# Performance work log

Measured on AMD Instinct MI355X. Metric: run time of the kernel, lower is better.

The kernel has to match this reference:

```python
import jax, jax.numpy as jnp
import numpy as np

N_AFFINES = 4
N_SDFS = 4
BATCH = 8192
DEPTH = 6


def setup_inputs() -> dict:
    key = jax.random.key(0)
    k1, k2, k3, k4, k5, k6, k7 = jax.random.split(key, 7)
    query = jax.random.normal(k1, (BATCH, 2), dtype=jnp.float32)
    # Contractive affines: scale*rotation + translation (homogeneous 3x3), guaranteed invertible.
    theta = jax.random.uniform(k2, (N_AFFINES,), minval=0.0, maxval=2.0 * np.pi)
    s = 0.4 + 0.2 * jax.random.uniform(k3, (N_AFFINES,))  # contraction factors in [0.4, 0.6]
    t = 0.4 * jax.random.normal(k4, (N_AFFINES, 2))
    c, sn = jnp.cos(theta), jnp.sin(theta)
    row0 = jnp.stack([s * c, -s * sn, t[:, 0]], axis=-1)
    row1 = jnp.stack([s * sn, s * c, t[:, 1]], axis=-1)
    row2 = jnp.broadcast_to(jnp.array([0.0, 0.0, 1.0]), (N_AFFINES, 3))
    affine_mats = jnp.stack([row0, row1, row2], axis=1).astype(jnp.float32)  # (N,3,3)
    sdf_centers = 0.5 * jax.random.normal(k5, (N_SDFS, 2), dtype=jnp.float32)
    sdf_radii = (0.3 + 0.2 * jax.random.uniform(k6, (N_SDFS,))).astype(jnp.float32)
    return {
        "query": query,
        "affine_scales": s.astype(jnp.float32),
        "affine_mats": affine_mats,
        "sdf_centers": sdf_centers,
        "sdf_radii": sdf_radii,
        "depth": DEPTH,
    }


def reference(query, affine_scales, affine_mats, sdf_centers, sdf_radii, depth):
    # back transforms: inverse matrices and reciprocal scales
    back_scales = 1.0 / affine_scales              # (N,)
    back_mats = jnp.linalg.inv(affine_mats)        # (N,3,3)

    # Compose all N^depth transform combinations (mirrors the nested list comprehension).
    Tm = jnp.eye(3, dtype=jnp.float32)[None]       # (1,3,3)
    sc = jnp.ones((1,), dtype=jnp.float32)         # (1,)
    for _ in range(depth):
        Tm = jnp.einsum('aij,njk->anik', Tm, back_mats).reshape(-1, 3, 3)
        sc = (sc[:, None] * back_scales[None, :]).reshape(-1)
    # Tm: (T,3,3), sc: (T,) with T = N^depth

    B = query.shape[0]
    qpad = jnp.concatenate([query, jnp.ones((B, 1), dtype=query.dtype)], axis=1)  # (B,3)
    qt = jnp.einsum('tij,bj->tbi', Tm, qpad)[..., :2]  # (T,B,2)

    # Circle SDFs: ||p - center|| - radius, batched over all K sdfs -> (T,K,B)
    diff = qt[:, None, :, :] - sdf_centers[None, :, None, :]
    d = jnp.sqrt(jnp.sum(diff * diff, axis=-1)) - sdf_radii[None, :, None]
    d = d / sc[:, None, None]  # 1/scale * sdf(...)

    return jnp.min(jnp.min(d, axis=0), axis=0)  # (B,)
```

## Files before the change

kernel.cpp:

```cpp
#include <hip/hip_runtime.h>
#include <math.h>


#define NA 4
#define T_TOTAL 4096
#define BATCH 8192
#define TPB 256
#define TCHUNK 64
#define NCHUNK 64

__device__ __forceinline__ float fsqrt(float x) { return __builtin_amdgcn_sqrtf(x); }

__constant__ unsigned char LO_COMBO[64] = {
    0, 21, 42, 63,
    1, 4, 16,   2, 8, 32,   3, 12, 48,
    20, 17, 5,  22, 25, 37, 23, 29, 53,
    40, 34, 10, 41, 38, 26, 43, 46, 58,
    60, 51, 15, 61, 55, 31, 62, 59, 47,
    6, 9, 18, 24, 33, 36,
    7, 13, 19, 28, 49, 52,
    11, 14, 35, 44, 50, 56,
    27, 30, 39, 45, 54, 57
};


__device__ __forceinline__ void compute_inverses(const float* __restrict__ mats,
                                                 const float* __restrict__ scales,
                                                 float (*inv)[8], int tid) {
    if (tid < NA) {
        const int n = tid;
        float a = mats[n * 9 + 0], b = mats[n * 9 + 1], e = mats[n * 9 + 2];
        float c = mats[n * 9 + 3], d = mats[n * 9 + 4], f = mats[n * 9 + 5];
        float rd = 1.0f / (a * d - b * c);
        float i00 = d * rd, i01 = -b * rd, i10 = -c * rd, i11 = a * rd;
        inv[n][0] = i00; inv[n][1] = i01; inv[n][2] = i10; inv[n][3] = i11;
        inv[n][4] = -(i00 * e + i01 * f);
        inv[n][5] = -(i10 * e + i11 * f);
        inv[n][6] = scales[n];
        inv[n][7] = 0.0f;
    }
}

__device__ __forceinline__ void gen_transforms(const float (*inv)[8], float4 (*xf)[4],
                                               int hi, int tid, int nthreads,
                                               const float* __restrict__ centers,
                                               const float* __restrict__ radii) {
    for (int i = tid; i < TCHUNK; i += nthreads) {
        int t = hi * 64 + (int)LO_COMBO[i];
        int dg = (t >> 10) & 3;
        float m00 = inv[dg][0], m01 = inv[dg][1], m10 = inv[dg][2], m11 = inv[dg][3];
        float tx = inv[dg][4], ty = inv[dg][5], sp = inv[dg][6];
        #pragma unroll
        for (int s = 8; s >= 0; s -= 2) {
            dg = (t >> s) & 3;
            float b00 = inv[dg][0], b01 = inv[dg][1], b10 = inv[dg][2], b11 = inv[dg][3];
            float bx = inv[dg][4], by = inv[dg][5];
            float n00 = fmaf(m00, b00, m01 * b10);
            float n01 = fmaf(m00, b01, m01 * b11);
            float n10 = fmaf(m10, b00, m11 * b10);
            float n11 = fmaf(m10, b01, m11 * b11);
            float nx  = fmaf(m00, bx, fmaf(m01, by, tx));
            float ny  = fmaf(m10, bx, fmaf(m11, by, ty));
            m00 = n00; m01 = n01; m10 = n10; m11 = n11; tx = nx; ty = ny;
            sp *= inv[dg][6];
        }
        float R00 = m00 * sp, R01 = m01 * sp, R10 = m10 * sp, R11 = m11 * sp;
        #pragma unroll
        for (int k = 0; k < 4; ++k) {
            float ex = (tx - centers[2 * k + 0]) * sp;
            float ey = (ty - centers[2 * k + 1]) * sp;
            float wx = 2.0f * fmaf(R00, ex, R10 * ey);
            float wy = 2.0f * fmaf(R01, ex, R11 * ey);
            float ee = fmaf(ex, ex, ey * ey);
            xf[i][k] = make_float4(wx, wy, ee, radii[k] * sp);
        }
    }
}

template <int SZ>
__device__ __forceinline__ void group_eval(const float4 (*xf)[4], int slot,
                                           float qx0, float qy0, float qq0,
                                           float qx1, float qy1, float qq1,
                                           float* d0, float* d1) {
    float sm0[4], sm1[4], rsp[4];
    #pragma unroll
    for (int k = 0; k < 4; ++k) {
        float4 W = xf[slot][k];
        sm0[k] = fmaf(W.x, qx0, fmaf(W.y, qy0, W.z));
        sm1[k] = fmaf(W.x, qx1, fmaf(W.y, qy1, W.z));
        rsp[k] = W.w;
    }
    #pragma unroll
    for (int i = 1; i < SZ; ++i) {
        #pragma unroll
        for (int k = 0; k < 4; ++k) {
            float4 W = xf[slot + i][k];
            sm0[k] = fminf(sm0[k], fmaf(W.x, qx0, fmaf(W.y, qy0, W.z)));
            sm1[k] = fminf(sm1[k], fmaf(W.x, qx1, fmaf(W.y, qy1, W.z)));
        }
    }
    #pragma unroll
    for (int k = 0; k < 4; ++k) {
        d0[k] = fminf(d0[k], fsqrt(fmaxf(sm0[k] + qq0, 0.0f)) - rsp[k]);
        d1[k] = fminf(d1[k], fsqrt(fmaxf(sm1[k] + qq1, 0.0f)) - rsp[k]);
    }
}

__device__ __forceinline__ void accum_grouped(const float4 (*xf)[4],
                                              float qx0, float qy0, float qq0,
                                              float qx1, float qy1, float qq1,
                                              float* d0, float* d1) {
    #pragma unroll
    for (int a = 0; a < 4; ++a)
        group_eval<1>(xf, a, qx0, qy0, qq0, qx1, qy1, qq1, d0, d1);
    #pragma unroll 4
    for (int m = 0; m < 12; ++m)
        group_eval<3>(xf, 4 + 3 * m, qx0, qy0, qq0, qx1, qy1, qq1, d0, d1);
    #pragma unroll
    for (int q = 0; q < 4; ++q)
        group_eval<6>(xf, 40 + 6 * q, qx0, qy0, qq0, qx1, qy1, qq1, d0, d1);
}


__global__ __launch_bounds__(TPB) void ifs_partial(const float* __restrict__ query,
                                                   const float* __restrict__ scales,
                                                   const float* __restrict__ mats,
                                                   const float* __restrict__ centers,
                                                   const float* __restrict__ radii,
                                                   float* __restrict__ partial) {
    __shared__ float inv[NA][8];
    __shared__ float4 xf[TCHUNK][4];
    const int tid = threadIdx.x;

    compute_inverses(mats, scales, inv, tid);
    __syncthreads();

    gen_transforms(inv, xf, blockIdx.y, tid, TPB, centers, radii);
    __syncthreads();

    const int pb = blockIdx.x * TPB + tid;
    float4 qq = ((const float4*)query)[pb];
    float qq0 = fmaf(qq.x, qq.x, qq.y * qq.y);
    float qq1 = fmaf(qq.z, qq.z, qq.w * qq.w);

    float d0[4] = {INFINITY, INFINITY, INFINITY, INFINITY};
    float d1[4] = {INFINITY, INFINITY, INFINITY, INFINITY};
    accum_grouped(xf, qq.x, qq.y, qq0, qq.z, qq.w, qq1, d0, d1);

    float p0 = fminf(fminf(d0[0], d0[1]), fminf(d0[2], d0[3]));
    float p1 = fminf(fminf(d1[0], d1[1]), fminf(d1[2], d1[3]));
    ((float2*)(partial + blockIdx.y * BATCH))[pb] = make_float2(p0, p1);
}

__global__ __launch_bounds__(TPB) void ifs_reduce(const float* __restrict__ partial,
                                                  float* __restrict__ out) {
    const int b = blockIdx.x * TPB + threadIdx.x;
    float m = INFINITY;
    #pragma unroll
    for (int c = 0; c < NCHUNK; ++c) m = fminf(m, partial[c * BATCH + b]);
    out[b] = m;
}

__global__ __launch_bounds__(TPB) void ifs_mono(const float* __restrict__ query,
                                                const float* __restrict__ scales,
                                                const float* __restrict__ mats,
                                                const float* __restrict__ centers,
                                                const float* __restrict__ radii,
                                                float* __restrict__ out) {
    __shared__ float inv[NA][8];
    __shared__ float4 xf[TCHUNK][4];
    const int tid = threadIdx.x;

    compute_inverses(mats, scales, inv, tid);
    __syncthreads();

    const int pb = blockIdx.x * TPB + tid;
    float4 qv = ((const float4*)query)[pb];
    float qq0 = fmaf(qv.x, qv.x, qv.y * qv.y);
    float qq1 = fmaf(qv.z, qv.z, qv.w * qv.w);

    float d0[4] = {INFINITY, INFINITY, INFINITY, INFINITY};
    float d1[4] = {INFINITY, INFINITY, INFINITY, INFINITY};
    for (int hi = 0; hi < NCHUNK; ++hi) {
        __syncthreads();
        gen_transforms(inv, xf, hi, tid, TPB, centers, radii);
        __syncthreads();
        accum_grouped(xf, qv.x, qv.y, qq0, qv.z, qv.w, qq1, d0, d1);
    }
    float p0 = fminf(fminf(d0[0], d0[1]), fminf(d0[2], d0[3]));
    float p1 = fminf(fminf(d1[0], d1[1]), fminf(d1[2], d1[3]));
    ((float2*)out)[pb] = make_float2(p0, p1);
}


extern "C" void kernel_launch(void* const* d_in, const int* in_sizes, int n_in,
                              void* d_out, int out_size, void* d_ws, size_t ws_size,
                              hipStream_t stream) {
    const float* query   = (const float*)d_in[0];
    const float* scales  = (const float*)d_in[1];
    const float* mats    = (const float*)d_in[2];
    const float* centers = (const float*)d_in[3];
    const float* radii   = (const float*)d_in[4];
    float* out = (float*)d_out;

    const size_t needed = (size_t)NCHUNK * BATCH * sizeof(float);

    if (ws_size >= needed) {
        float* partial = (float*)d_ws;
        dim3 grid(BATCH / (TPB * 2), NCHUNK);
        ifs_partial<<<grid, TPB, 0, stream>>>(query, scales, mats, centers,
                                              radii, partial);
        ifs_reduce<<<BATCH / TPB, TPB, 0, stream>>>(partial, out);
    } else {
        ifs_mono<<<BATCH / (TPB * 2), TPB, 0, stream>>>(query, scales, mats, centers,
                                                        radii, out);
    }
}
```

Baseline: 82.90 us.

## Process eight query points per thread to amortize LDS transform loads

The partial kernel now handles eight query points per thread (up from two) with 128-thread blocks, so each float4 transform read from shared memory is reused across eight points. The grouped loops are no longer unrolled, which limits code size and register growth. The grid shrinks to 8x64 blocks, and each block still regenerates its chunk of transforms. The trade-off is fewer waves in flight and higher register pressure in exchange for less LDS traffic per FLOP.

```diff
diff --git a/kernel.cpp b/kernel.cpp
--- a/kernel.cpp
+++ b/kernel.cpp
@@ -5,9 +5,10 @@
 #define NA 4
 #define T_TOTAL 4096
 #define BATCH 8192
-#define TPB 256
+#define TPB 128
 #define TCHUNK 64
 #define NCHUNK 64
+#define PPL 8
 
 __device__ __forceinline__ float fsqrt(float x) { return __builtin_amdgcn_sqrtf(x); }
 
@@ -78,56 +79,58 @@
 }
 
 template <int SZ>
-__device__ __forceinline__ void group_eval(const float4 (*xf)[4], int slot,
-                                           float qx0, float qy0, float qq0,
-                                           float qx1, float qy1, float qq1,
-                                           float* d0, float* d1) {
-    float sm0[4], sm1[4], rsp[4];
+__device__ __forceinline__ void group_eval8(const float4 (*xf)[4], int slot,
+                                            const float* qx, const float* qy,
+                                            const float* qq, float* d) {
+    float sm[PPL][4];
+    float rsp[4];
     #pragma unroll
     for (int k = 0; k < 4; ++k) {
         float4 W = xf[slot][k];
-        sm0[k] = fmaf(W.x, qx0, fmaf(W.y, qy0, W.z));
-        sm1[k] = fmaf(W.x, qx1, fmaf(W.y, qy1, W.z));
         rsp[k] = W.w;
+        #pragma unroll
+        for (int p = 0; p < PPL; ++p)
+            sm[p][k] = fmaf(W.x, qx[p], fmaf(W.y, qy[p], W.z));
     }
     #pragma unroll
     for (int i = 1; i < SZ; ++i) {
         #pragma unroll
         for (int k = 0; k < 4; ++k) {
             float4 W = xf[slot + i][k];
-            sm0[k] = fminf(sm0[k], fmaf(W.x, qx0, fmaf(W.y, qy0, W.z)));
-            sm1[k] = fminf(sm1[k], fmaf(W.x, qx1, fmaf(W.y, qy1, W.z)));
-        }
-    }
-    #pragma unroll
-    for (int k = 0; k < 4; ++k) {
-        d0[k] = fminf(d0[k], fsqrt(fmaxf(sm0[k] + qq0, 0.0f)) - rsp[k]);
-        d1[k] = fminf(d1[k], fsqrt(fmaxf(sm1[k] + qq1, 0.0f)) - rsp[k]);
-    }
-}
-
-__device__ __forceinline__ void accum_grouped(const float4 (*xf)[4],
-                                              float qx0, float qy0, float qq0,
-                                              float qx1, float qy1, float qq1,
-                                              float* d0, float* d1) {
-    #pragma unroll
+            #pragma unroll
+            for (int p = 0; p < PPL; ++p)
+                sm[p][k] = fminf(sm[p][k], fmaf(W.x, qx[p], fmaf(W.y, qy[p], W.z)));
+        }
+    }
+    #pragma unroll
+    for (int p = 0; p < PPL; ++p) {
+        #pragma unroll
+        for (int k = 0; k < 4; ++k)
+            d[p] = fminf(d[p], fsqrt(fmaxf(sm[p][k] + qq[p], 0.0f)) - rsp[k]);
+    }
+}
+
+__device__ __forceinline__ void accum_grouped8(const float4 (*xf)[4],
+                                               const float* qx, const float* qy,
+                                               const float* qq, float* d) {
+    #pragma unroll 1
     for (int a = 0; a < 4; ++a)
-        group_eval<1>(xf, a, qx0, qy0, qq0, qx1, qy1, qq1, d0, d1);
-    #pragma unroll 4
+        group_eval8<1>(xf, a, qx, qy, qq, d);
+    #pragma unroll 1
     for (int m = 0; m < 12; ++m)
-        group_eval<3>(xf, 4 + 3 * m, qx0, qy0, qq0, qx1, qy1, qq1, d0, d1);
-    #pragma unroll
-    for (int q = 0; q < 4; ++q)
-        group_eval<6>(xf, 40 + 6 * q, qx0, qy0, qq0, qx1, qy1, qq1, d0, d1);
-}
-
-
-__global__ __launch_bounds__(TPB) void ifs_partial(const float* __restrict__ query,
-                                                   const float* __restrict__ scales,
-                                                   const float* __restrict__ mats,
-                                                   const float* __restrict__ centers,
-                                                   const float* __restrict__ radii,
-                                                   float* __restrict__ partial) {
+        group_eval8<3>(xf, 4 + 3 * m, qx, qy, qq, d);
+    #pragma unroll 1
+    for (int g = 0; g < 4; ++g)
+        group_eval8<6>(xf, 40 + 6 * g, qx, qy, qq, d);
+}
+
+
+__global__ __launch_bounds__(TPB) void ifs_partial8(const float* __restrict__ query,
+                                                    const float* __restrict__ scales,
+                                                    const float* __restrict__ mats,
+                                                    const float* __restrict__ centers,
+                                                    const float* __restrict__ radii,
+                                                    float* __restrict__ partial) {
     __shared__ float inv[NA][8];
     __shared__ float4 xf[TCHUNK][4];
     const int tid = threadIdx.x;
@@ -138,30 +141,35 @@
     gen_transforms(inv, xf, blockIdx.y, tid, TPB, centers, radii);
     __syncthreads();
 
-    const int pb = blockIdx.x * TPB + tid;
-    float4 qq = ((const float4*)query)[pb];
-    float qq0 = fmaf(qq.x, qq.x, qq.y * qq.y);
-    float qq1 = fmaf(qq.z, qq.z, qq.w * qq.w);
-
-    float d0[4] = {INFINITY, INFINITY, INFINITY, INFINITY};
-    float d1[4] = {INFINITY, INFINITY, INFINITY, INFINITY};
-    accum_grouped(xf, qq.x, qq.y, qq0, qq.z, qq.w, qq1, d0, d1);
-
-    float p0 = fminf(fminf(d0[0], d0[1]), fminf(d0[2], d0[3]));
-    float p1 = fminf(fminf(d1[0], d1[1]), fminf(d1[2], d1[3]));
-    ((float2*)(partial + blockIdx.y * BATCH))[pb] = make_float2(p0, p1);
-}
-
-__global__ __launch_bounds__(TPB) void ifs_reduce(const float* __restrict__ partial,
+    const int base = blockIdx.x * (PPL * TPB) + tid;
+    const float2* q2 = (const float2*)query;
+
+    float qx[PPL], qy[PPL], qq[PPL], d[PPL];
+    #pragma unroll
+    for (int p = 0; p < PPL; ++p) {
+        float2 q = q2[base + p * TPB];
+        qx[p] = q.x; qy[p] = q.y;
+        qq[p] = fmaf(q.x, q.x, q.y * q.y);
+        d[p] = INFINITY;
+    }
+
+    accum_grouped8(xf, qx, qy, qq, d);
+
+    float* prow = partial + blockIdx.y * BATCH + base;
+    #pragma unroll
+    for (int p = 0; p < PPL; ++p) prow[p * TPB] = d[p];
+}
+
+__global__ __launch_bounds__(256) void ifs_reduce(const float* __restrict__ partial,
                                                   float* __restrict__ out) {
-    const int b = blockIdx.x * TPB + threadIdx.x;
+    const int b = blockIdx.x * 256 + threadIdx.x;
     float m = INFINITY;
     #pragma unroll
     for (int c = 0; c < NCHUNK; ++c) m = fminf(m, partial[c * BATCH + b]);
     out[b] = m;
 }
 
-__global__ __launch_bounds__(TPB) void ifs_mono(const float* __restrict__ query,
+__global__ __launch_bounds__(256) void ifs_mono(const float* __restrict__ query,
                                                 const float* __restrict__ scales,
                                                 const float* __restrict__ mats,
                                                 const float* __restrict__ centers,
@@ -174,22 +182,84 @@
     compute_inverses(mats, scales, inv, tid);
     __syncthreads();
 
-    const int pb = blockIdx.x * TPB + tid;
+    const int pb = blockIdx.x * 256 + tid;
     float4 qv = ((const float4*)query)[pb];
-    float qq0 = fmaf(qv.x, qv.x, qv.y * qv.y);
-    float qq1 = fmaf(qv.z, qv.z, qv.w * qv.w);
-
-    float d0[4] = {INFINITY, INFINITY, INFINITY, INFINITY};
-    float d1[4] = {INFINITY, INFINITY, INFINITY, INFINITY};
+    float qx[2] = {qv.x, qv.z}, qy[2] = {qv.y, qv.w};
+    float qq[2] = {fmaf(qv.x, qv.x, qv.y * qv.y), fmaf(qv.z, qv.z, qv.w * qv.w)};
+    float d[2] = {INFINITY, INFINITY};
+
     for (int hi = 0; hi < NCHUNK; ++hi) {
         __syncthreads();
-        gen_transforms(inv, xf, hi, tid, TPB, centers, radii);
+        gen_transforms(inv, xf, hi, tid, 256, centers, radii);
         __syncthreads();
-        accum_grouped(xf, qv.x, qv.y, qq0, qv.z, qv.w, qq1, d0, d1);
-    }
-    float p0 = fminf(fminf(d0[0], d0[1]), fminf(d0[2], d0[3]));
-    float p1 = fminf(fminf(d1[0], d1[1]), fminf(d1[2], d1[3]));
-    ((float2*)out)[pb] = make_float2(p0, p1);
+        float sm[2][4], rsp[4];
+        #pragma unroll 1
+        for (int a = 0; a < 4; ++a) {
+            #pragma unroll
+            for (int k = 0; k < 4; ++k) {
+                float4 W = xf[a][k]; rsp[k] = W.w;
+                #pragma unroll
+                for (int p = 0; p < 2; ++p)
+                    sm[p][k] = fmaf(W.x, qx[p], fmaf(W.y, qy[p], W.z));
+            }
+            #pragma unroll
+            for (int p = 0; p < 2; ++p)
+                #pragma unroll
+                for (int k = 0; k < 4; ++k)
+                    d[p] = fminf(d[p], fsqrt(fmaxf(sm[p][k] + qq[p], 0.0f)) - rsp[k]);
+        }
+        #pragma unroll 1
+        for (int m = 0; m < 12; ++m) {
+            int slot = 4 + 3 * m;
+            #pragma unroll
+            for (int k = 0; k < 4; ++k) {
+                float4 W = xf[slot][k]; rsp[k] = W.w;
+                #pragma unroll
+                for (int p = 0; p < 2; ++p)
+                    sm[p][k] = fmaf(W.x, qx[p], fmaf(W.y, qy[p], W.z));
+            }
+            #pragma unroll
+            for (int i = 1; i < 3; ++i)
+                #pragma unroll
+                for (int k = 0; k < 4; ++k) {
+                    float4 W = xf[slot + i][k];
+                    #pragma unroll
+                    for (int p = 0; p < 2; ++p)
+                        sm[p][k] = fminf(sm[p][k], fmaf(W.x, qx[p], fmaf(W.y, qy[p], W.z)));
+                }
+            #pragma unroll
+            for (int p = 0; p < 2; ++p)
+                #pragma unroll
+                for (int k = 0; k < 4; ++k)
+                    d[p] = fminf(d[p], fsqrt(fmaxf(sm[p][k] + qq[p], 0.0f)) - rsp[k]);
+        }
+        #pragma unroll 1
+        for (int g = 0; g < 4; ++g) {
+            int slot = 40 + 6 * g;
+            #pragma unroll
+            for (int k = 0; k < 4; ++k) {
+                float4 W = xf[slot][k]; rsp[k] = W.w;
+                #pragma unroll
+                for (int p = 0; p < 2; ++p)
+                    sm[p][k] = fmaf(W.x, qx[p], fmaf(W.y, qy[p], W.z));
+            }
+            #pragma unroll
+            for (int i = 1; i < 6; ++i)
+                #pragma unroll
+                for (int k = 0; k < 4; ++k) {
+                    float4 W = xf[slot + i][k];
+                    #pragma unroll
+                    for (int p = 0; p < 2; ++p)
+                        sm[p][k] = fminf(sm[p][k], fmaf(W.x, qx[p], fmaf(W.y, qy[p], W.z)));
+                }
+            #pragma unroll
+            for (int p = 0; p < 2; ++p)
+                #pragma unroll
+                for (int k = 0; k < 4; ++k)
+                    d[p] = fminf(d[p], fsqrt(fmaxf(sm[p][k] + qq[p], 0.0f)) - rsp[k]);
+        }
+    }
+    ((float2*)out)[pb] = make_float2(d[0], d[1]);
 }
 
 
@@ -207,12 +277,12 @@
 
     if (ws_size >= needed) {
         float* partial = (float*)d_ws;
-        dim3 grid(BATCH / (TPB * 2), NCHUNK);
-        ifs_partial<<<grid, TPB, 0, stream>>>(query, scales, mats, centers,
-                                              radii, partial);
-        ifs_reduce<<<BATCH / TPB, TPB, 0, stream>>>(partial, out);
+        dim3 grid(BATCH / (TPB * PPL), NCHUNK);
+        ifs_partial8<<<grid, TPB, 0, stream>>>(query, scales, mats, centers,
+                                               radii, partial);
+        ifs_reduce<<<BATCH / 256, 256, 0, stream>>>(partial, out);
     } else {
-        ifs_mono<<<BATCH / (TPB * 2), TPB, 0, stream>>>(query, scales, mats, centers,
+        ifs_mono<<<BATCH / (256 * 2), 256, 0, stream>>>(query, scales, mats, centers,
                                                         radii, out);
     }
 }
```

Result: slower. 94.59 us (+14.1%).
